# Optimization experiments

Hardware: AMD Instinct MI355X
Metric: run time of the kernel (lower is better)

The kernel has to match this reference:

```python
import jax, jax.numpy as jnp
import numpy as np

IN_COUNT = 1024
OUT_COUNT = 1024
NUM_BASIS = 8
INPUT_ABS_MAX = 1.0
X_MIN = 0.0
X_MAX = 1.0
GAMMA_SCALE = 3.0
BATCH = 4096


def setup_inputs() -> dict:
    key = jax.random.key(0)
    k_x, k_c = jax.random.split(key)
    x = jax.random.normal(k_x, (BATCH, IN_COUNT), dtype=jnp.float32)
    coeffs = 0.01 * jax.random.normal(k_c, (OUT_COUNT, IN_COUNT, NUM_BASIS), dtype=jnp.float32)
    # fixed buffers
    centers_1d = jnp.linspace(X_MIN, X_MAX, NUM_BASIS)
    centers = jnp.broadcast_to(centers_1d[None, :], (IN_COUNT, NUM_BASIS)).astype(jnp.float32)
    delta = (X_MAX - X_MIN) / (NUM_BASIS - 1)
    gamma = GAMMA_SCALE / delta
    slopes = jnp.full((IN_COUNT, NUM_BASIS), gamma, dtype=jnp.float32)
    alpha = jnp.full((IN_COUNT,), (X_MAX - X_MIN) / (2.0 * INPUT_ABS_MAX), dtype=jnp.float32)
    beta = jnp.full((IN_COUNT,), 0.5 * (X_MIN + X_MAX), dtype=jnp.float32)
    return {"x": x, "coeffs": coeffs, "centers": centers, "slopes": slopes, "alpha": alpha, "beta": beta}


def reference(x, coeffs, centers, slopes, alpha, beta):
    # u: (B, in) affine transform with fixed alpha/beta
    u = alpha[None, :] * x + beta[None, :]
    # basis: (B, in, basis) = 0.5*(1+tanh(slope*(u - center)))
    basis = 0.5 * (1.0 + jnp.tanh(slopes[None, :, :] * (u[:, :, None] - centers[None, :, :])))
    # y[b,o] = sum_{i,m} coeffs[o,i,m] * basis[b,i,m]  (fused GEMM over in*basis)
    y = jnp.einsum('bim,oim->bo', basis, coeffs)
    return y
```

## Files before the change

kernel.cpp:

```cpp
#include <hip/hip_runtime.h>
#include <hip/hip_bf16.h>
#include <cstdint>
#include <cstddef>

#define BATCH 4096
#define INC   1024
#define OUTC  1024
#define NB    8
#define KDIM  (INC * NB)

#define BM 128
#define BN 128
#define BKB 128
#define SPLITS 4
#define KSPLIT (KDIM / SPLITS)

typedef int  v4i __attribute__((ext_vector_type(4)));
typedef char v8c __attribute__((ext_vector_type(8)));

__device__ __forceinline__ void gld16(const char* g, char* l) {
  __builtin_amdgcn_global_load_lds(
      (const __attribute__((address_space(1))) unsigned int*)g,
      (__attribute__((address_space(3))) unsigned int*)l, 16, 0, 0);
}

__global__ __launch_bounds__(256) void expand_kernel(
    const float* __restrict__ x, const float* __restrict__ centers,
    const float* __restrict__ slopes, const float* __restrict__ alpha,
    const float* __restrict__ beta, char* __restrict__ Ai8) {
  const int idx = blockIdx.x * 256 + threadIdx.x;
  const int i = idx & (INC - 1);
  const float u = alpha[i] * x[idx] + beta[i];
  const float s0 = slopes[i * NB];
  const float c0 = centers[i * NB];
  const float c1 = centers[i * NB + 1];
  const float L2E2 = 2.8853900817779268f;
  const float a2 = L2E2 * s0;
  float e = __builtin_amdgcn_exp2f(a2 * (c0 - u));
  const float R = __builtin_amdgcn_exp2f(a2 * (c1 - c0));
  v8c q;
#pragma unroll
  for (int m = 0; m < 8; ++m) {
    float basis = __builtin_amdgcn_rcpf(1.0f + e);
    q[m] = (char)(int)rintf(basis * 254.0f - 127.0f);
    e *= R;
  }
  *(v8c*)(Ai8 + (size_t)idx * 8) = q;
}

__global__ __launch_bounds__(256) void rowstat_kernel(
    const float4* __restrict__ coeffs4, float* __restrict__ maxrow) {
  const int o = blockIdx.x;
  const int tid = threadIdx.x;
  const float4* row = coeffs4 + (size_t)o * (KDIM / 4);
  float m = 0.0f;
  for (int t = tid; t < KDIM / 4; t += 256) {
    float4 v = row[t];
    m = fmaxf(m, fmaxf(fmaxf(fabsf(v.x), fabsf(v.y)), fmaxf(fabsf(v.z), fabsf(v.w))));
  }
#pragma unroll
  for (int off = 32; off; off >>= 1) m = fmaxf(m, __shfl_xor(m, off));
  __shared__ float wm[4];
  if ((tid & 63) == 0) wm[tid >> 6] = m;
  __syncthreads();
  if (tid == 0)
    maxrow[o] = fmaxf(fmaxf(fmaxf(wm[0], wm[1]), fmaxf(wm[2], wm[3])), 1e-30f);
}

__global__ __launch_bounds__(256) void convert_kernel(
    const float4* __restrict__ coeffs4, const float* __restrict__ maxrow,
    int* __restrict__ Ci8_as_int, int* __restrict__ qcsum) {
  const int idx4 = blockIdx.x * 256 + threadIdx.x;
  const int o = idx4 >> 11;
  const float s = 127.0f / maxrow[o];
  float4 v = coeffs4[idx4];
  int q0 = (int)rintf(v.x * s), q1 = (int)rintf(v.y * s);
  int q2 = (int)rintf(v.z * s), q3 = (int)rintf(v.w * s);
  Ci8_as_int[idx4] = (q0 & 0xFF) | ((q1 & 0xFF) << 8) | ((q2 & 0xFF) << 16) | (q3 << 24);
  int qs = q0 + q1 + q2 + q3;
#pragma unroll
  for (int off = 32; off; off >>= 1) qs += __shfl_xor(qs, off);
  __shared__ int ws4[4];
  const int tid = threadIdx.x;
  if ((tid & 63) == 0) ws4[tid >> 6] = qs;
  __syncthreads();
  if (tid == 0) atomicAdd(&qcsum[o], ws4[0] + ws4[1] + ws4[2] + ws4[3]);
}

__global__ __launch_bounds__(256) void gemm_kernel(
    const char* __restrict__ A, const char* __restrict__ C,
    int* __restrict__ partials) {
  __shared__ char As[BM * BKB];
  __shared__ char Bs[BN * BKB];

  const int id = blockIdx.x;
  const int z  = id >> 8;
  const int p  = id & 255;
  const int st = p >> 6;
  const int q  = p & 63;
  const int bx = q & 7;
  const int by = st * 8 + (q >> 3);
  const int bn0 = bx * BN;
  const int bm0 = by * BM;

  const int tid  = threadIdx.x;
  const int wave = tid >> 6;
  const int lane = tid & 63;
  const int quad = lane >> 4;
  const int lm   = lane & 15;
  const int wm = (wave & 1) * 64;
  const int wn = (wave >> 1) * 64;
  const int kt0 = z * KSPLIT;
  int* out = partials + (size_t)z * BATCH * OUTC;

  const int r_in = lane >> 3;
  const int kg   = (lane & 7) ^ r_in;

  const char* pA[4];
  const char* pB[4];
  char* lA[4];
  char* lB[4];
#pragma unroll
  for (int j = 0; j < 4; ++j) {
    const int rb = wave * 32 + j * 8;
    pA[j] = A + (size_t)(bm0 + rb + r_in) * KDIM + kt0 + kg * 16;
    pB[j] = C + (size_t)(bn0 + rb + r_in) * KDIM + kt0 + kg * 16;
    lA[j] = As + rb * BKB;
    lB[j] = Bs + rb * BKB;
  }

  v4i acc[4][4] = {};

  for (int it = 0; it < KSPLIT / BKB; ++it) {
#pragma unroll
    for (int j = 0; j < 4; ++j) {
      gld16(pA[j], lA[j]);
      gld16(pB[j], lB[j]);
      pA[j] += BKB; pB[j] += BKB;
    }
    __syncthreads();

#pragma unroll
    for (int kp = 0; kp < 2; ++kp) {
      v4i a[4], b[4];
#pragma unroll
      for (int fm = 0; fm < 4; ++fm) {
        const int row = wm + fm * 16 + lm;
        const int kgs = (kp * 4 + quad) ^ (row & 7);
        a[fm] = *(const v4i*)(As + row * BKB + kgs * 16);
      }
#pragma unroll
      for (int fn = 0; fn < 4; ++fn) {
        const int row = wn + fn * 16 + lm;
        const int kgs = (kp * 4 + quad) ^ (row & 7);
        b[fn] = *(const v4i*)(Bs + row * BKB + kgs * 16);
      }
#pragma unroll
      for (int fm = 0; fm < 4; ++fm)
#pragma unroll
        for (int fn = 0; fn < 4; ++fn)
          acc[fm][fn] = __builtin_amdgcn_mfma_i32_16x16x64_i8(a[fm], b[fn], acc[fm][fn], 0, 0, 0);
    }
    __syncthreads();
  }

#pragma unroll
  for (int fm = 0; fm < 4; ++fm) {
    const int row0 = bm0 + wm + fm * 16 + quad * 4;
#pragma unroll
    for (int fn = 0; fn < 4; ++fn) {
      const int col = bn0 + wn + fn * 16 + lm;
#pragma unroll
      for (int r = 0; r < 4; ++r)
        out[(size_t)(row0 + r) * OUTC + col] = acc[fm][fn][r];
    }
  }
}

__global__ __launch_bounds__(256) void reduce_kernel(
    const int4* __restrict__ P, const float4* __restrict__ maxrow4,
    const int4* __restrict__ qcsum4, float4* __restrict__ out) {
  const size_t n4 = (size_t)BATCH * OUTC / 4;
  const size_t idx4 = (size_t)blockIdx.x * 256 + threadIdx.x;
  int4 s = P[idx4];
#pragma unroll
  for (int t = 1; t < SPLITS; ++t) {
    int4 v = P[(size_t)t * n4 + idx4];
    s.x += v.x; s.y += v.y; s.z += v.z; s.w += v.w;
  }
  const int o4 = (int)(idx4 & (OUTC / 4 - 1));
  float4 M = maxrow4[o4];
  int4  Q = qcsum4[o4];
  const float inv = 1.0f / 32258.0f;
  float4 y;
  y.x = M.x * (float)(s.x + 127 * Q.x) * inv;
  y.y = M.y * (float)(s.y + 127 * Q.y) * inv;
  y.z = M.z * (float)(s.z + 127 * Q.z) * inv;
  y.w = M.w * (float)(s.w + 127 * Q.w) * inv;
  out[idx4] = y;
}

extern "C" void kernel_launch(void* const* d_in, const int* in_sizes, int n_in,
                              void* d_out, int out_size, void* d_ws, size_t ws_size,
                              hipStream_t stream) {
  const float* x       = (const float*)d_in[0];
  const float* coeffs  = (const float*)d_in[1];
  const float* centers = (const float*)d_in[2];
  const float* slopes  = (const float*)d_in[3];
  const float* alpha   = (const float*)d_in[4];
  const float* beta    = (const float*)d_in[5];
  float* out = (float*)d_out;

  const size_t a_bytes = (size_t)BATCH * KDIM;
  const size_t c_bytes = (size_t)OUTC * KDIM;
  const size_t stat_bytes = OUTC * sizeof(float);
  const size_t qcs_bytes  = OUTC * sizeof(int);
  const size_t part_bytes = (size_t)SPLITS * BATCH * OUTC * sizeof(int);
  if (ws_size < a_bytes + c_bytes + stat_bytes + qcs_bytes + part_bytes) return;

  char*  Ai8    = (char*)d_ws;
  char*  Ci8    = Ai8 + a_bytes;
  float* maxrow = (float*)(Ci8 + c_bytes);
  int*   qcsum  = (int*)((char*)maxrow + stat_bytes);
  int*   parts  = (int*)((char*)qcsum + qcs_bytes);

  expand_kernel<<<(BATCH * INC) / 256, 256, 0, stream>>>(
      x, centers, slopes, alpha, beta, Ai8);

  rowstat_kernel<<<OUTC, 256, 0, stream>>>((const float4*)coeffs, maxrow);

  hipMemsetAsync(qcsum, 0, qcs_bytes, stream);

  convert_kernel<<<(OUTC * KDIM / 4) / 256, 256, 0, stream>>>(
      (const float4*)coeffs, maxrow, (int*)Ci8, qcsum);

  gemm_kernel<<<(OUTC / BN) * (BATCH / BM) * SPLITS, 256, 0, stream>>>(
      Ai8, Ci8, parts);

  reduce_kernel<<<(int)((size_t)BATCH * OUTC / 4 / 256), 256, 0, stream>>>(
      (const int4*)parts, (const float4*)maxrow, (const int4*)qcsum, (float4*)out);
}
```

Before: 186.8 us.

## Fuse prep kernels into one launch and store split-K partials as bf16

Merges the input expansion, coefficient row-max and coefficient quantization into a single prep kernel. Each coefficient row is now read once and kept in registers for both the max and the quantize pass, which removes the memset and the atomics. The GEMM writes split-K partials as bf16 instead of int32, halving partial-sum traffic for the write and for the reduce read. The bf16 partials lose precision on the integer accumulators, which risks larger output error.

```diff
diff --git a/kernel.cpp b/kernel.cpp
--- a/kernel.cpp
+++ b/kernel.cpp
@@ -15,8 +15,22 @@
 #define SPLITS 4
 #define KSPLIT (KDIM / SPLITS)
 
-typedef int  v4i __attribute__((ext_vector_type(4)));
-typedef char v8c __attribute__((ext_vector_type(8)));
+#define EXPAND_BLOCKS  ((BATCH * INC) / 256)
+#define QUANT_BLOCKS   OUTC
+#define PREP_BLOCKS    (EXPAND_BLOCKS + QUANT_BLOCKS)
+
+typedef int   v4i __attribute__((ext_vector_type(4)));
+typedef char  v8c __attribute__((ext_vector_type(8)));
+typedef short v8s __attribute__((ext_vector_type(8)));
+
+__device__ __forceinline__ unsigned short f2bf(float f) {
+  union { float f; unsigned u; } v; v.f = f;
+  unsigned r = v.u + 0x7fffu + ((v.u >> 16) & 1u);
+  return (unsigned short)(r >> 16);
+}
+__device__ __forceinline__ float bf2f(unsigned short h) {
+  union { unsigned u; float f; } v; v.u = ((unsigned)h) << 16; return v.f;
+}
 
 __device__ __forceinline__ void gld16(const char* g, char* l) {
   __builtin_amdgcn_global_load_lds(
@@ -24,72 +38,72 @@
       (__attribute__((address_space(3))) unsigned int*)l, 16, 0, 0);
 }
 
-__global__ __launch_bounds__(256) void expand_kernel(
-    const float* __restrict__ x, const float* __restrict__ centers,
-    const float* __restrict__ slopes, const float* __restrict__ alpha,
-    const float* __restrict__ beta, char* __restrict__ Ai8) {
-  const int idx = blockIdx.x * 256 + threadIdx.x;
-  const int i = idx & (INC - 1);
-  const float u = alpha[i] * x[idx] + beta[i];
-  const float s0 = slopes[i * NB];
-  const float c0 = centers[i * NB];
-  const float c1 = centers[i * NB + 1];
-  const float L2E2 = 2.8853900817779268f;
-  const float a2 = L2E2 * s0;
-  float e = __builtin_amdgcn_exp2f(a2 * (c0 - u));
-  const float R = __builtin_amdgcn_exp2f(a2 * (c1 - c0));
-  v8c q;
-#pragma unroll
-  for (int m = 0; m < 8; ++m) {
-    float basis = __builtin_amdgcn_rcpf(1.0f + e);
-    q[m] = (char)(int)rintf(basis * 254.0f - 127.0f);
-    e *= R;
-  }
-  *(v8c*)(Ai8 + (size_t)idx * 8) = q;
-}
-
-__global__ __launch_bounds__(256) void rowstat_kernel(
-    const float4* __restrict__ coeffs4, float* __restrict__ maxrow) {
-  const int o = blockIdx.x;
+__global__ __launch_bounds__(256) void prep_kernel(
+    const float* __restrict__ x, const float4* __restrict__ coeffs4,
+    const float* __restrict__ centers, const float* __restrict__ slopes,
+    const float* __restrict__ alpha, const float* __restrict__ beta,
+    char* __restrict__ Ai8, int* __restrict__ Ci8i,
+    float* __restrict__ maxrow, int* __restrict__ qcsum) {
+  const int blk = blockIdx.x;
   const int tid = threadIdx.x;
-  const float4* row = coeffs4 + (size_t)o * (KDIM / 4);
-  float m = 0.0f;
-  for (int t = tid; t < KDIM / 4; t += 256) {
-    float4 v = row[t];
-    m = fmaxf(m, fmaxf(fmaxf(fabsf(v.x), fabsf(v.y)), fmaxf(fabsf(v.z), fabsf(v.w))));
-  }
-#pragma unroll
-  for (int off = 32; off; off >>= 1) m = fmaxf(m, __shfl_xor(m, off));
-  __shared__ float wm[4];
-  if ((tid & 63) == 0) wm[tid >> 6] = m;
-  __syncthreads();
-  if (tid == 0)
-    maxrow[o] = fmaxf(fmaxf(fmaxf(wm[0], wm[1]), fmaxf(wm[2], wm[3])), 1e-30f);
-}
-
-__global__ __launch_bounds__(256) void convert_kernel(
-    const float4* __restrict__ coeffs4, const float* __restrict__ maxrow,
-    int* __restrict__ Ci8_as_int, int* __restrict__ qcsum) {
-  const int idx4 = blockIdx.x * 256 + threadIdx.x;
-  const int o = idx4 >> 11;
-  const float s = 127.0f / maxrow[o];
-  float4 v = coeffs4[idx4];
-  int q0 = (int)rintf(v.x * s), q1 = (int)rintf(v.y * s);
-  int q2 = (int)rintf(v.z * s), q3 = (int)rintf(v.w * s);
-  Ci8_as_int[idx4] = (q0 & 0xFF) | ((q1 & 0xFF) << 8) | ((q2 & 0xFF) << 16) | (q3 << 24);
-  int qs = q0 + q1 + q2 + q3;
-#pragma unroll
-  for (int off = 32; off; off >>= 1) qs += __shfl_xor(qs, off);
-  __shared__ int ws4[4];
-  const int tid = threadIdx.x;
-  if ((tid & 63) == 0) ws4[tid >> 6] = qs;
-  __syncthreads();
-  if (tid == 0) atomicAdd(&qcsum[o], ws4[0] + ws4[1] + ws4[2] + ws4[3]);
+  if (blk < EXPAND_BLOCKS) {
+    const int idx = blk * 256 + tid;
+    const int i = idx & (INC - 1);
+    const float u = alpha[i] * x[idx] + beta[i];
+    const float s0 = slopes[i * NB];
+    const float c0 = centers[i * NB];
+    const float c1 = centers[i * NB + 1];
+    const float L2E2 = 2.8853900817779268f;
+    const float a2 = L2E2 * s0;
+    float e = __builtin_amdgcn_exp2f(a2 * (c0 - u));
+    const float R = __builtin_amdgcn_exp2f(a2 * (c1 - c0));
+    v8c q;
+#pragma unroll
+    for (int m = 0; m < 8; ++m) {
+      float basis = __builtin_amdgcn_rcpf(1.0f + e);
+      q[m] = (char)(int)rintf(basis * 254.0f - 127.0f);
+      e *= R;
+    }
+    *(v8c*)(Ai8 + (size_t)idx * 8) = q;
+  } else {
+    const int o = blk - EXPAND_BLOCKS;
+    const float4* row = coeffs4 + (size_t)o * (KDIM / 4);
+    float4 v[8];
+    float m = 0.0f;
+#pragma unroll
+    for (int j = 0; j < 8; ++j) {
+      v[j] = row[tid + 256 * j];
+      m = fmaxf(m, fmaxf(fmaxf(fabsf(v[j].x), fabsf(v[j].y)),
+                         fmaxf(fabsf(v[j].z), fabsf(v[j].w))));
+    }
+#pragma unroll
+    for (int off = 32; off; off >>= 1) m = fmaxf(m, __shfl_xor(m, off));
+    __shared__ float wm[4];
+    __shared__ int   wq[4];
+    if ((tid & 63) == 0) wm[tid >> 6] = m;
+    __syncthreads();
+    const float M = fmaxf(fmaxf(fmaxf(wm[0], wm[1]), fmaxf(wm[2], wm[3])), 1e-30f);
+    const float s = 127.0f / M;
+    int qs = 0;
+#pragma unroll
+    for (int j = 0; j < 8; ++j) {
+      int q0 = (int)rintf(v[j].x * s), q1 = (int)rintf(v[j].y * s);
+      int q2 = (int)rintf(v[j].z * s), q3 = (int)rintf(v[j].w * s);
+      Ci8i[(size_t)o * (KDIM / 4) + tid + 256 * j] =
+          (q0 & 0xFF) | ((q1 & 0xFF) << 8) | ((q2 & 0xFF) << 16) | ((q3 & 0xFF) << 24);
+      qs += q0 + q1 + q2 + q3;
+    }
+#pragma unroll
+    for (int off = 32; off; off >>= 1) qs += __shfl_xor(qs, off);
+    if ((tid & 63) == 0) wq[tid >> 6] = qs;
+    __syncthreads();
+    if (tid == 0) { maxrow[o] = M; qcsum[o] = wq[0] + wq[1] + wq[2] + wq[3]; }
+  }
 }
 
 __global__ __launch_bounds__(256) void gemm_kernel(
     const char* __restrict__ A, const char* __restrict__ C,
-    int* __restrict__ partials) {
+    unsigned short* __restrict__ partials) {
   __shared__ char As[BM * BKB];
   __shared__ char Bs[BN * BKB];
 
@@ -111,7 +125,7 @@
   const int wm = (wave & 1) * 64;
   const int wn = (wave >> 1) * 64;
   const int kt0 = z * KSPLIT;
-  int* out = partials + (size_t)z * BATCH * OUTC;
+  unsigned short* out = partials + (size_t)z * BATCH * OUTC;
 
   const int r_in = lane >> 3;
   const int kg   = (lane & 7) ^ r_in;
@@ -172,32 +186,33 @@
       const int col = bn0 + wn + fn * 16 + lm;
 #pragma unroll
       for (int r = 0; r < 4; ++r)
-        out[(size_t)(row0 + r) * OUTC + col] = acc[fm][fn][r];
+        out[(size_t)(row0 + r) * OUTC + col] = f2bf((float)acc[fm][fn][r]);
     }
   }
 }
 
 __global__ __launch_bounds__(256) void reduce_kernel(
-    const int4* __restrict__ P, const float4* __restrict__ maxrow4,
-    const int4* __restrict__ qcsum4, float4* __restrict__ out) {
-  const size_t n4 = (size_t)BATCH * OUTC / 4;
-  const size_t idx4 = (size_t)blockIdx.x * 256 + threadIdx.x;
-  int4 s = P[idx4];
-#pragma unroll
-  for (int t = 1; t < SPLITS; ++t) {
-    int4 v = P[(size_t)t * n4 + idx4];
-    s.x += v.x; s.y += v.y; s.z += v.z; s.w += v.w;
-  }
-  const int o4 = (int)(idx4 & (OUTC / 4 - 1));
-  float4 M = maxrow4[o4];
-  int4  Q = qcsum4[o4];
+    const unsigned short* __restrict__ P, const float* __restrict__ maxrow,
+    const int* __restrict__ qcsum, float* __restrict__ out) {
+  const size_t nel = (size_t)BATCH * OUTC;
+  const size_t base = ((size_t)blockIdx.x * 256 + threadIdx.x) * 8;
+  float s[8] = {};
+#pragma unroll
+  for (int t = 0; t < SPLITS; ++t) {
+    v8s v = *(const v8s*)(P + t * nel + base);
+#pragma unroll
+    for (int j = 0; j < 8; ++j) s[j] += bf2f((unsigned short)v[j]);
+  }
+  const int o0 = (int)(base & (OUTC - 1));
   const float inv = 1.0f / 32258.0f;
-  float4 y;
-  y.x = M.x * (float)(s.x + 127 * Q.x) * inv;
-  y.y = M.y * (float)(s.y + 127 * Q.y) * inv;
-  y.z = M.z * (float)(s.z + 127 * Q.z) * inv;
-  y.w = M.w * (float)(s.w + 127 * Q.w) * inv;
-  out[idx4] = y;
+#pragma unroll
+  for (int j = 0; j < 8; ++j) {
+    const float M = maxrow[o0 + j];
+    const int   Q = qcsum[o0 + j];
+    s[j] = M * (s[j] + 127.0f * (float)Q) * inv;
+  }
+  *(float4*)(out + base)     = float4{s[0], s[1], s[2], s[3]};
+  *(float4*)(out + base + 4) = float4{s[4], s[5], s[6], s[7]};
 }
 
 extern "C" void kernel_launch(void* const* d_in, const int* in_sizes, int n_in,
@@ -211,32 +226,26 @@
   const float* beta    = (const float*)d_in[5];
   float* out = (float*)d_out;
 
-  const size_t a_bytes = (size_t)BATCH * KDIM;
-  const size_t c_bytes = (size_t)OUTC * KDIM;
+  const size_t a_bytes    = (size_t)BATCH * KDIM;
+  const size_t c_bytes    = (size_t)OUTC * KDIM;
   const size_t stat_bytes = OUTC * sizeof(float);
   const size_t qcs_bytes  = OUTC * sizeof(int);
-  const size_t part_bytes = (size_t)SPLITS * BATCH * OUTC * sizeof(int);
+  const size_t part_bytes = (size_t)SPLITS * BATCH * OUTC * 2;
   if (ws_size < a_bytes + c_bytes + stat_bytes + qcs_bytes + part_bytes) return;
 
   char*  Ai8    = (char*)d_ws;
   char*  Ci8    = Ai8 + a_bytes;
   float* maxrow = (float*)(Ci8 + c_bytes);
   int*   qcsum  = (int*)((char*)maxrow + stat_bytes);
-  int*   parts  = (int*)((char*)qcsum + qcs_bytes);
-
-  expand_kernel<<<(BATCH * INC) / 256, 256, 0, stream>>>(
-      x, centers, slopes, alpha, beta, Ai8);
-
-  rowstat_kernel<<<OUTC, 256, 0, stream>>>((const float4*)coeffs, maxrow);
-
-  hipMemsetAsync(qcsum, 0, qcs_bytes, stream);
-
-  convert_kernel<<<(OUTC * KDIM / 4) / 256, 256, 0, stream>>>(
-      (const float4*)coeffs, maxrow, (int*)Ci8, qcsum);
+  unsigned short* parts = (unsigned short*)((char*)qcsum + qcs_bytes);
+
+  prep_kernel<<<PREP_BLOCKS, 256, 0, stream>>>(
+      x, (const float4*)coeffs, centers, slopes, alpha, beta,
+      Ai8, (int*)Ci8, maxrow, qcsum);
 
   gemm_kernel<<<(OUTC / BN) * (BATCH / BM) * SPLITS, 256, 0, stream>>>(
       Ai8, Ci8, parts);
 
-  reduce_kernel<<<(int)((size_t)BATCH * OUTC / 4 / 256), 256, 0, stream>>>(
-      (const int4*)parts, (const float4*)maxrow, (const int4*)qcsum, (float4*)out);
-}
+  reduce_kernel<<<(int)((size_t)BATCH * OUTC / 8 / 256), 256, 0, stream>>>(
+      parts, maxrow, qcsum, out);
+}
```

After: 164.7 us. 11.8% less time.
